# Performance work log

Measured on AMD Instinct MI355X. Metric: run time of the kernel, lower is better.

## Reference

```python
import jax, jax.numpy as jnp
import numpy as np

B, N, E = 16, 576, 768
H, HID = 12, 768
D = HID // H          # dim_head = 64
SCALE = D ** -0.5
LN_EPS = 1e-5


def setup_inputs() -> dict:
    key = jax.random.key(0)
    ks = jax.random.split(key, 12)
    x = jax.random.normal(ks[0], (B, N, E), jnp.float32)
    dist = jax.random.uniform(ks[1], (N, N), jnp.float32) * 24.0  # pairwise patch distances
    s = E ** -0.5
    return {
        "x": x,
        "dist": dist,
        "ln_g": jnp.ones((E,), jnp.float32),
        "ln_b": jnp.zeros((E,), jnp.float32),
        "Wq": jax.random.normal(ks[2], (E, HID), jnp.float32) * s,
        "bq": jnp.zeros((HID,), jnp.float32),
        "Wk": jax.random.normal(ks[3], (E, HID), jnp.float32) * s,
        "bk": jnp.zeros((HID,), jnp.float32),
        "Wv": jax.random.normal(ks[4], (E, HID), jnp.float32) * s,
        "bv": jnp.zeros((HID,), jnp.float32),
        "Wo": jax.random.normal(ks[5], (HID, E), jnp.float32) * (HID ** -0.5),
        "bo": jnp.zeros((E,), jnp.float32),
        "ak": jax.random.normal(ks[6], (D,), jnp.float32) * 0.1,
        "av": jax.random.normal(ks[7], (D,), jnp.float32) * 0.1,
    }


def _rpe(a, dist):
    # MonotonicallyDecreasingFunctionParallel: per-channel learned decay rate,
    # out[i,j,c] = exp(-softplus(a_c) * dist[i,j])  ->  [N, N, D]
    rate = jax.nn.softplus(a)
    return jnp.exp(-dist[:, :, None] * rate[None, None, :])


def reference(x, dist, ln_g, ln_b, Wq, bq, Wk, bk, Wv, bv, Wo, bo, ak, av):
    b, n = x.shape[0], x.shape[1]
    # LayerNorm
    mu = jnp.mean(x, axis=-1, keepdims=True)
    var = jnp.mean(jnp.square(x - mu), axis=-1, keepdims=True)
    xn = (x - mu) * jax.lax.rsqrt(var + LN_EPS) * ln_g + ln_b
    # projections, then raw row-major reshape [B, H, n, d] (faithful to .view)
    q = (xn @ Wq + bq).reshape(b, H, n, D)
    k = (xn @ Wk + bk).reshape(b, H, n, D)
    v = (xn @ Wv + bv).reshape(b, H, n, D)
    QKT = jnp.einsum("bhnd,bhmd->bhnm", q, k)
    rel_k = _rpe(ak, dist)  # [n, n, D]
    rel_v = _rpe(av, dist)  # [n, n, D]
    # faithful raw reshape [B,H,n,d] -> [n, B*H, d]
    q_r = q.reshape(n, b * H, D)
    QAT = jnp.einsum("nbd,nmd->nbm", q_r, rel_k).reshape(b, H, n, n)
    attn = jax.nn.softmax((QKT + QAT) * SCALE, axis=-1)
    attn_V = jnp.einsum("bhnm,bhmd->bhnd", attn, v)
    attn_r = attn.reshape(n, b * H, n)
    attn_rel_v = jnp.einsum("nbm,nmd->nbd", attn_r, rel_v).reshape(b, H, n, D)
    out = (attn_V + attn_rel_v).reshape(b, n, HID)
    out = out @ Wo + bo  # dropout is identity in eval mode
    return out
```

## Files before the change

### kernel.cpp

```cpp
#include <hip/hip_runtime.h>
#include <hip/hip_fp16.h>

typedef _Float16 f16;
typedef _Float16 v8hf __attribute__((ext_vector_type(8)));
typedef float v4f __attribute__((ext_vector_type(4)));
typedef float v16f __attribute__((ext_vector_type(16)));
typedef unsigned int v4u __attribute__((ext_vector_type(4)));

#define NROW 9216
#define SZH ((size_t)NROW * 768)

__device__ __forceinline__ float softplus_f(float a) {
  return fmaxf(a, 0.f) + log1pf(__expf(-fabsf(a)));
}

__device__ __forceinline__ unsigned int packh(float a, float b) {
  union { f16 h[2]; unsigned int u; } z;
  z.h[0] = (f16)a; z.h[1] = (f16)b;
  return z.u;
}

__global__ __launch_bounds__(256) void prep_kernel(
    const float* __restrict__ x, const float* __restrict__ lg, const float* __restrict__ lb,
    const float* __restrict__ Wq, const float* __restrict__ Wk, const float* __restrict__ Wv,
    const float* __restrict__ Wo, const float* __restrict__ ak, const float* __restrict__ av,
    const float* __restrict__ bq, const float* __restrict__ bk, const float* __restrict__ bv,
    f16* __restrict__ xn, f16* __restrict__ wt, float* __restrict__ biasqkv,
    float* __restrict__ rates)
{
  __shared__ float tile[64][65];
  __shared__ float red[8];
  int bid = blockIdx.x, tid = threadIdx.x;
  if (bid < NROW) {
    const float* xr = x + (size_t)bid * 768;
    float v0 = xr[tid], v1 = xr[tid + 256], v2 = xr[tid + 512];
    float s1 = v0 + v1 + v2;
    float s2 = v0 * v0 + v1 * v1 + v2 * v2;
    #pragma unroll
    for (int off = 32; off >= 1; off >>= 1) {
      s1 += __shfl_xor(s1, off);
      s2 += __shfl_xor(s2, off);
    }
    int w = tid >> 6;
    if ((tid & 63) == 0) { red[w] = s1; red[4 + w] = s2; }
    __syncthreads();
    s1 = red[0] + red[1] + red[2] + red[3];
    s2 = red[4] + red[5] + red[6] + red[7];
    float mu = s1 * (1.f / 768.f);
    float var = s2 * (1.f / 768.f) - mu * mu;
    float rs = rsqrtf(var + 1e-5f);
    f16* xo = xn + (size_t)bid * 768;
    xo[tid]       = (f16)((v0 - mu) * rs * lg[tid] + lb[tid]);
    xo[tid + 256] = (f16)((v1 - mu) * rs * lg[tid + 256] + lb[tid + 256]);
    xo[tid + 512] = (f16)((v2 - mu) * rs * lg[tid + 512] + lb[tid + 512]);
    return;
  }
  bid -= NROW;
  if (bid < 576) {
    int wsel = bid / 144, t2 = bid % 144, tr = t2 / 12, tc = t2 % 12;
    const float* W = (wsel == 0) ? Wq : ((wsel == 1) ? Wk : ((wsel == 2) ? Wv : Wo));
    f16* WT = wt + (size_t)wsel * 589824;
    int r = tid >> 2, c0 = (tid & 3) * 16;
    #pragma unroll
    for (int j = 0; j < 16; j++)
      tile[r][c0 + j] = W[(size_t)(tr * 64 + r) * 768 + tc * 64 + c0 + j];
    __syncthreads();
    #pragma unroll
    for (int j = 0; j < 16; j++)
      WT[(size_t)(tc * 64 + r) * 768 + tr * 64 + c0 + j] = (f16)tile[c0 + j][r];
    return;
  }
  if (tid < 64) rates[tid] = softplus_f(ak[tid]);
  else if (tid < 128) rates[tid] = softplus_f(av[tid - 64]);
  for (int i = tid; i < 2304; i += 256)
    biasqkv[i] = (i < 768) ? bq[i] : ((i < 1536) ? bk[i - 768] : bv[i - 1536]);
}

__global__ __launch_bounds__(256) void gemm_kernel(
    const f16* __restrict__ A, const f16* __restrict__ WT,
    const float* __restrict__ bias,
    f16* __restrict__ outh, float* __restrict__ outf, int f32out)
{
  __shared__ __align__(16) f16 At[128 * 64];
  __shared__ __align__(16) f16 Bt[128 * 64];
  int mb = blockIdx.x, nb = blockIdx.y;
  int tid = threadIdx.x, lane = tid & 63, w = tid >> 6;
  int wr = w >> 1, wc = w & 1;
  v4f acc[4][4];
  #pragma unroll
  for (int i = 0; i < 4; i++)
    #pragma unroll
    for (int j = 0; j < 4; j++) acc[i][j] = (v4f){0.f, 0.f, 0.f, 0.f};
  int arow0 = mb * 128, brow0 = nb * 128;
  for (int ks = 0; ks < 12; ++ks) {
    int k0 = ks * 64;
    #pragma unroll
    for (int qq = 0; qq < 4; ++qq) {
      int o = (qq * 256 + tid) * 16;
      int row = o >> 7, bc = o & 127;
      int dst = row * 128 + (bc ^ ((row & 7) << 4));
      *(v8hf*)((char*)At + dst) = *(const v8hf*)(A + (size_t)(arow0 + row) * 768 + k0 + (bc >> 1));
      *(v8hf*)((char*)Bt + dst) = *(const v8hf*)(WT + (size_t)(brow0 + row) * 768 + k0 + (bc >> 1));
    }
    __syncthreads();
    v8hf bf[4][2];
    #pragma unroll
    for (int cf = 0; cf < 4; cf++)
      #pragma unroll
      for (int kk = 0; kk < 2; kk++) {
        int row = wc * 64 + cf * 16 + (lane & 15);
        int bc = kk * 64 + ((lane >> 4) << 4);
        bf[cf][kk] = *(const v8hf*)((char*)Bt + row * 128 + (bc ^ ((row & 7) << 4)));
      }
    #pragma unroll
    for (int rf = 0; rf < 4; rf++) {
      v8hf af[2];
      int row = wr * 64 + rf * 16 + (lane & 15);
      #pragma unroll
      for (int kk = 0; kk < 2; kk++) {
        int bc = kk * 64 + ((lane >> 4) << 4);
        af[kk] = *(const v8hf*)((char*)At + row * 128 + (bc ^ ((row & 7) << 4)));
      }
      #pragma unroll
      for (int cf = 0; cf < 4; cf++) {
        acc[rf][cf] = __builtin_amdgcn_mfma_f32_16x16x32_f16(af[0], bf[cf][0], acc[rf][cf], 0, 0, 0);
        acc[rf][cf] = __builtin_amdgcn_mfma_f32_16x16x32_f16(af[1], bf[cf][1], acc[rf][cf], 0, 0, 0);
      }
    }
    __syncthreads();
  }
  #pragma unroll
  for (int cf = 0; cf < 4; cf++) {
    int col = nb * 128 + wc * 64 + cf * 16 + (lane & 15);
    float bb = bias[col];
    int z = col / 768;
    int colz = col - z * 768;
    #pragma unroll
    for (int rf = 0; rf < 4; rf++) {
      int row0 = mb * 128 + wr * 64 + rf * 16 + ((lane >> 4) << 2);
      #pragma unroll
      for (int r = 0; r < 4; r++) {
        float val = acc[rf][cf][r] + bb;
        if (f32out) outf[(size_t)(row0 + r) * 768 + col] = val;
        else outh[(size_t)z * SZH + (size_t)(row0 + r) * 768 + colz] = (f16)val;
      }
    }
  }
}

__global__ __launch_bounds__(256) void vt_kernel(const f16* __restrict__ vw, f16* __restrict__ vt)
{
  __shared__ f16 tile[64][72];
  int g = blockIdx.x, tc = blockIdx.y;
  int tid = threadIdx.x;
  int tr = tid >> 2, c16 = (tid & 3) * 16;
  const f16* src = vw + (size_t)g * 36864 + (size_t)(tc * 64 + tr) * 64 + c16;
  *(v8hf*)&tile[tr][c16] = *(const v8hf*)src;
  *(v8hf*)&tile[tr][c16 + 8] = *(const v8hf*)(src + 8);
  __syncthreads();
  int d = tid >> 2, t16 = (tid & 3) * 16;
  f16 outv[16];
  #pragma unroll
  for (int j = 0; j < 16; j++) outv[j] = tile[t16 + j][d];
  f16* dst = vt + (size_t)g * 36864 + (size_t)d * 576 + tc * 64 + t16;
  *(v8hf*)dst = *(v8hf*)outv;
  *(v8hf*)(dst + 8) = *(v8hf*)(outv + 8);
}

__global__ __launch_bounds__(384, 3) void attn_kernel(
    const f16* __restrict__ qw, const f16* __restrict__ kw, const f16* __restrict__ vt,
    const float* __restrict__ dist, const float* __restrict__ rates,
    f16* __restrict__ aw, float* __restrict__ part, float* __restrict__ ml, int nslice)
{
  __shared__ __align__(16) f16 Ke[64 * 64];
  __shared__ __align__(16) f16 Vt[64 * 64];
  __shared__ float dl[576];
  __shared__ float rkv[128];
  int gc = blockIdx.x;
  int sl = blockIdx.y;
  int g = gc / 3, c = gc - g * 3;
  int tid = threadIdx.x, lane = tid & 63, w = tid >> 6;
  int l31 = lane & 31, h = lane >> 5;
  int ntile = 9 / nslice;
  size_t hbase = (size_t)g * 36864;
  if (tid < 128) rkv[tid] = rates[tid];
  for (int t = tid; t < ntile * 64; t += 384)
    dl[t] = dist[(size_t)gc * 576 + sl * ntile * 64 + t];
  __syncthreads();
  v8hf qf[4];
  {
    const f16* qp = qw + hbase + (size_t)(c * 192 + w * 32 + l31) * 64 + h * 8;
    #pragma unroll
    for (int kk = 0; kk < 4; kk++) {
      v8hf v = *(const v8hf*)(qp + kk * 16);
      #pragma unroll
      for (int j = 0; j < 8; j++) v[j] = v[j] * (f16)0.125f;
      qf[kk] = v;
    }
  }
  v16f o0 = {0}, o1 = {0};
  #pragma unroll
  for (int i = 0; i < 16; i++) { o0[i] = 0.f; o1[i] = 0.f; }
  float mrun = -1e30f, lrun = 0.f;
  for (int t = 0; t < ntile; ++t) {
    int mbase = sl * ntile * 64 + t * 64;
    int mloc = t * 64;
    for (int u = tid; u < 1024; u += 384) {
      if (u < 512) {
        int mm = u >> 3, d8 = (u & 7) * 8;
        float dv = dl[mloc + mm];
        v8hf kv = *(const v8hf*)(kw + hbase + (size_t)(mbase + mm) * 64 + d8);
        #pragma unroll
        for (int j = 0; j < 8; j++)
          kv[j] = (f16)((float)kv[j] + __expf(-rkv[d8 + j] * dv));
        *(v8hf*)((char*)Ke + mm * 128 + ((d8 * 2) ^ ((mm & 7) << 4))) = kv;
      } else {
        int uu = u - 512;
        int dd = uu >> 3, m8 = (uu & 7) * 8;
        float rv = rkv[64 + dd];
        v8hf vv = *(const v8hf*)(vt + hbase + (size_t)dd * 576 + mbase + m8);
        #pragma unroll
        for (int j = 0; j < 8; j++)
          vv[j] = (f16)((float)vv[j] + __expf(-rv * dl[mloc + m8 + j]));
        *(v8hf*)((char*)Vt + dd * 128 + ((m8 * 2) ^ ((dd & 7) << 4))) = vv;
      }
    }
    __syncthreads();
    v16f s0 = {0}, s1 = {0};
    #pragma unroll
    for (int i = 0; i < 16; i++) { s0[i] = 0.f; s1[i] = 0.f; }
    #pragma unroll
    for (int kk = 0; kk < 4; kk++) {
      int bc = kk * 32 + h * 16;
      int sw0 = (l31 & 7) << 4;
      v8hf a0 = *(const v8hf*)((char*)Ke + l31 * 128 + (bc ^ sw0));
      v8hf a1 = *(const v8hf*)((char*)Ke + (32 + l31) * 128 + (bc ^ sw0));
      s0 = __builtin_amdgcn_mfma_f32_32x32x16_f16(a0, qf[kk], s0, 0, 0, 0);
      s1 = __builtin_amdgcn_mfma_f32_32x32x16_f16(a1, qf[kk], s1, 0, 0, 0);
    }
    float tmax = s0[0];
    #pragma unroll
    for (int i = 1; i < 16; i++) tmax = fmaxf(tmax, s0[i]);
    #pragma unroll
    for (int i = 0; i < 16; i++) tmax = fmaxf(tmax, s1[i]);
    tmax = fmaxf(tmax, __shfl_xor(tmax, 32));
    float mnew = fmaxf(mrun, tmax);
    float alpha = __expf(mrun - mnew);
    float rs = 0.f;
    #pragma unroll
    for (int i = 0; i < 16; i++) { float p = __expf(s0[i] - mnew); s0[i] = p; rs += p; }
    #pragma unroll
    for (int i = 0; i < 16; i++) { float p = __expf(s1[i] - mnew); s1[i] = p; rs += p; }
    rs += __shfl_xor(rs, 32);
    lrun = lrun * alpha + rs;
    mrun = mnew;
    #pragma unroll
    for (int i = 0; i < 16; i++) { o0[i] *= alpha; o1[i] *= alpha; }
    unsigned int Wd[16], Xd[16];
    #pragma unroll
    for (int i = 0; i < 8; i++) {
      Wd[i]     = packh(s0[2 * i], s0[2 * i + 1]);
      Wd[8 + i] = packh(s1[2 * i], s1[2 * i + 1]);
    }
    #pragma unroll
    for (int i = 0; i < 16; i++) Xd[i] = __shfl_xor((int)Wd[i], 32);
    v4u fw[4];
    fw[0] = h ? (v4u){Xd[2],  Xd[3],  Wd[2],  Wd[3]}  : (v4u){Wd[0],  Wd[1],  Xd[0],  Xd[1]};
    fw[1] = h ? (v4u){Xd[6],  Xd[7],  Wd[6],  Wd[7]}  : (v4u){Wd[4],  Wd[5],  Xd[4],  Xd[5]};
    fw[2] = h ? (v4u){Xd[10], Xd[11], Wd[10], Wd[11]} : (v4u){Wd[8],  Wd[9],  Xd[8],  Xd[9]};
    fw[3] = h ? (v4u){Xd[14], Xd[15], Wd[14], Wd[15]} : (v4u){Wd[12], Wd[13], Xd[12], Xd[13]};
    #pragma unroll
    for (int kk = 0; kk < 4; kk++) {
      int bc = kk * 32 + h * 16;
      int sw0 = (l31 & 7) << 4;
      v8hf a0 = *(const v8hf*)((char*)Vt + l31 * 128 + (bc ^ sw0));
      v8hf a1 = *(const v8hf*)((char*)Vt + (32 + l31) * 128 + (bc ^ sw0));
      union { v4u u; v8hf hh; } pb;
      pb.u = fw[kk];
      o0 = __builtin_amdgcn_mfma_f32_32x32x16_f16(a0, pb.hh, o0, 0, 0, 0);
      o1 = __builtin_amdgcn_mfma_f32_32x32x16_f16(a1, pb.hh, o1, 0, 0, 0);
    }
    __syncthreads();
  }
  if (nslice == 1) {
    float inv = 1.f / lrun;
    f16* ap = aw + hbase + (size_t)(c * 192 + w * 32 + l31) * 64;
    #pragma unroll
    for (int r = 0; r < 16; r++) {
      int d = (r & 3) + 8 * (r >> 2) + 4 * h;
      ap[d]      = (f16)(o0[r] * inv);
      ap[d + 32] = (f16)(o1[r] * inv);
    }
  } else {
    float* pp = part + ((size_t)sl * 576 + gc) * 12288;
    int q = w * 32 + l31;
    #pragma unroll
    for (int r = 0; r < 16; r++) {
      int d = (r & 3) + 8 * (r >> 2) + 4 * h;
      pp[d * 192 + q]        = o0[r];
      pp[(d + 32) * 192 + q] = o1[r];
    }
    if (h == 0) {
      float* mlp = ml + ((size_t)sl * 576 + gc) * 384;
      mlp[q]       = mrun;
      mlp[192 + q] = lrun;
    }
  }
}

__global__ __launch_bounds__(192) void comb_kernel(
    const float* __restrict__ part, const float* __restrict__ ml, f16* __restrict__ aw)
{
  int gc = blockIdx.x;
  int q = threadIdx.x;
  int g = gc / 3, c = gc - g * 3;
  float mv[3], lv[3];
  float M = -1e30f;
  #pragma unroll
  for (int s = 0; s < 3; s++) {
    const float* mlp = ml + ((size_t)s * 576 + gc) * 384;
    mv[s] = mlp[q];
    lv[s] = mlp[192 + q];
    M = fmaxf(M, mv[s]);
  }
  float L = 0.f, sc[3];
  #pragma unroll
  for (int s = 0; s < 3; s++) { sc[s] = __expf(mv[s] - M); L += lv[s] * sc[s]; }
  float inv = 1.f / L;
  f16 row[64];
  #pragma unroll
  for (int d = 0; d < 64; d++) {
    float a = 0.f;
    #pragma unroll
    for (int s = 0; s < 3; s++)
      a += part[((size_t)s * 576 + gc) * 12288 + d * 192 + q] * sc[s];
    row[d] = (f16)(a * inv);
  }
  f16* ap = aw + (size_t)g * 36864 + (size_t)(c * 192 + q) * 64;
  #pragma unroll
  for (int j = 0; j < 8; j++) *(v8hf*)(ap + j * 8) = *(v8hf*)(row + j * 8);
}

extern "C" void kernel_launch(void* const* d_in, const int* in_sizes, int n_in,
                              void* d_out, int out_size, void* d_ws, size_t ws_size,
                              hipStream_t stream) {
  const float* x    = (const float*)d_in[0];
  const float* dist = (const float*)d_in[1];
  const float* lg   = (const float*)d_in[2];
  const float* lb   = (const float*)d_in[3];
  const float* Wq   = (const float*)d_in[4];
  const float* bq   = (const float*)d_in[5];
  const float* Wk   = (const float*)d_in[6];
  const float* bk   = (const float*)d_in[7];
  const float* Wv   = (const float*)d_in[8];
  const float* bv   = (const float*)d_in[9];
  const float* Wo   = (const float*)d_in[10];
  const float* bo   = (const float*)d_in[11];
  const float* ak   = (const float*)d_in[12];
  const float* av   = (const float*)d_in[13];

  f16* ws = (f16*)d_ws;
  f16* xn = ws;
  f16* qw = ws + SZH;
  f16* kw = ws + 2 * SZH;
  f16* vw = ws + 3 * SZH;
  f16* wt = ws + 4 * SZH;
  float* fbase   = (float*)(ws + 4 * SZH + 4 * 589824);
  float* biasqkv = fbase;
  float* rates   = fbase + 2304;
  float* part    = fbase + 2432;
  float* mlb     = part + (size_t)3 * 576 * 12288;
  f16* vtb = xn;
  f16* aw  = vw;

  size_t need_split = ((size_t)(4 * SZH + 4 * 589824) * 2) + 4 * (2432 + (size_t)3 * 576 * 12288 + (size_t)3 * 576 * 384);
  int ns = (ws_size >= need_split) ? 3 : 1;

  prep_kernel<<<9216 + 576 + 1, 256, 0, stream>>>(x, lg, lb, Wq, Wk, Wv, Wo, ak, av,
                                                  bq, bk, bv, xn, wt, biasqkv, rates);
  gemm_kernel<<<dim3(72, 18), 256, 0, stream>>>(xn, wt, biasqkv, qw, nullptr, 0);
  vt_kernel<<<dim3(192, 9), 256, 0, stream>>>(vw, vtb);
  attn_kernel<<<dim3(576, ns), 384, 0, stream>>>(qw, kw, vtb, dist, rates, aw, part, mlb, ns);
  if (ns > 1)
    comb_kernel<<<576, 192, 0, stream>>>(part, mlb, aw);
  gemm_kernel<<<dim3(72, 6), 256, 0, stream>>>(aw, wt + 3 * 589824, bo, nullptr, (float*)d_out, 1);
}
```

Baseline: 189.4 us.

## Use direct global-to-LDS loads, XCD-aware block remap, lazy softmax rescale, fp16 partials

The GEMM tile loads now use global_load_lds DMA instead of going through registers, and GEMM and attention workgroup indices are remapped so neighbouring tiles land on the same XCD. The online softmax skips the max and accumulator rescale unless the new tile max exceeds the running max by more than 8, which saves exponentials and multiplies. Split-K attention partials are normalised and stored as fp16 instead of fp32, halving combine traffic at some cost in precision. packh also switches to the cvt_pkrtz intrinsic.

```diff
diff --git a/kernel.cpp b/kernel.cpp
--- a/kernel.cpp
+++ b/kernel.cpp
@@ -3,6 +3,7 @@
 
 typedef _Float16 f16;
 typedef _Float16 v8hf __attribute__((ext_vector_type(8)));
+typedef __fp16 v2fp __attribute__((ext_vector_type(2)));
 typedef float v4f __attribute__((ext_vector_type(4)));
 typedef float v16f __attribute__((ext_vector_type(16)));
 typedef unsigned int v4u __attribute__((ext_vector_type(4)));
@@ -15,9 +16,16 @@
 }
 
 __device__ __forceinline__ unsigned int packh(float a, float b) {
-  union { f16 h[2]; unsigned int u; } z;
-  z.h[0] = (f16)a; z.h[1] = (f16)b;
+  union { v2fp h; unsigned int u; } z;
+  z.h = __builtin_amdgcn_cvt_pkrtz(a, b);
   return z.u;
+}
+
+__device__ __forceinline__ void gload16(const void* g, void* l) {
+  __builtin_amdgcn_global_load_lds(
+      (const __attribute__((address_space(1))) unsigned int*)(unsigned long long)g,
+      (__attribute__((address_space(3))) unsigned int*)(unsigned int)(unsigned long long)l,
+      16, 0, 0);
 }
 
 __global__ __launch_bounds__(256) void prep_kernel(
@@ -83,7 +91,11 @@
 {
   __shared__ __align__(16) f16 At[128 * 64];
   __shared__ __align__(16) f16 Bt[128 * 64];
-  int mb = blockIdx.x, nb = blockIdx.y;
+  int bid0 = blockIdx.y * gridDim.x + blockIdx.x;
+  int nwg = gridDim.x * gridDim.y;
+  int nid = (bid0 & 7) * (nwg >> 3) + (bid0 >> 3);
+  int cols = gridDim.y;
+  int mb = nid / cols, nb = nid % cols;
   int tid = threadIdx.x, lane = tid & 63, w = tid >> 6;
   int wr = w >> 1, wc = w & 1;
   v4f acc[4][4];
@@ -92,15 +104,16 @@
     #pragma unroll
     for (int j = 0; j < 4; j++) acc[i][j] = (v4f){0.f, 0.f, 0.f, 0.f};
   int arow0 = mb * 128, brow0 = nb * 128;
+  int rb = w * 32 + (lane >> 3);
+  int ch = lane & 7;
   for (int ks = 0; ks < 12; ++ks) {
     int k0 = ks * 64;
     #pragma unroll
-    for (int qq = 0; qq < 4; ++qq) {
-      int o = (qq * 256 + tid) * 16;
-      int row = o >> 7, bc = o & 127;
-      int dst = row * 128 + (bc ^ ((row & 7) << 4));
-      *(v8hf*)((char*)At + dst) = *(const v8hf*)(A + (size_t)(arow0 + row) * 768 + k0 + (bc >> 1));
-      *(v8hf*)((char*)Bt + dst) = *(const v8hf*)(WT + (size_t)(brow0 + row) * 768 + k0 + (bc >> 1));
+    for (int j = 0; j < 4; j++) {
+      int row = rb + j * 8;
+      int sc = ((ch ^ (row & 7)) << 3);
+      gload16(A  + (size_t)(arow0 + row) * 768 + k0 + sc, (char*)At + w * 4096 + j * 1024);
+      gload16(WT + (size_t)(brow0 + row) * 768 + k0 + sc, (char*)Bt + w * 4096 + j * 1024);
     }
     __syncthreads();
     v8hf bf[4][2];
@@ -170,13 +183,13 @@
 __global__ __launch_bounds__(384, 3) void attn_kernel(
     const f16* __restrict__ qw, const f16* __restrict__ kw, const f16* __restrict__ vt,
     const float* __restrict__ dist, const float* __restrict__ rates,
-    f16* __restrict__ aw, float* __restrict__ part, float* __restrict__ ml, int nslice)
+    f16* __restrict__ aw, f16* __restrict__ parth, float* __restrict__ ml, int nslice)
 {
   __shared__ __align__(16) f16 Ke[64 * 64];
   __shared__ __align__(16) f16 Vt[64 * 64];
   __shared__ float dl[576];
   __shared__ float rkv[128];
-  int gc = blockIdx.x;
+  int gc = (blockIdx.x & 7) * 72 + (blockIdx.x >> 3);
   int sl = blockIdx.y;
   int g = gc / 3, c = gc - g * 3;
   int tid = threadIdx.x, lane = tid & 63, w = tid >> 6;
@@ -198,7 +211,7 @@
       qf[kk] = v;
     }
   }
-  v16f o0 = {0}, o1 = {0};
+  v16f o0, o1;
   #pragma unroll
   for (int i = 0; i < 16; i++) { o0[i] = 0.f; o1[i] = 0.f; }
   float mrun = -1e30f, lrun = 0.f;
@@ -226,7 +239,7 @@
       }
     }
     __syncthreads();
-    v16f s0 = {0}, s1 = {0};
+    v16f s0, s1;
     #pragma unroll
     for (int i = 0; i < 16; i++) { s0[i] = 0.f; s1[i] = 0.f; }
     #pragma unroll
@@ -244,18 +257,21 @@
     #pragma unroll
     for (int i = 0; i < 16; i++) tmax = fmaxf(tmax, s1[i]);
     tmax = fmaxf(tmax, __shfl_xor(tmax, 32));
-    float mnew = fmaxf(mrun, tmax);
-    float alpha = __expf(mrun - mnew);
+    if (!__all(tmax - mrun <= 8.f)) {
+      float mnew = fmaxf(mrun, tmax);
+      float alpha = __expf(mrun - mnew);
+      lrun *= alpha;
+      #pragma unroll
+      for (int i = 0; i < 16; i++) { o0[i] *= alpha; o1[i] *= alpha; }
+      mrun = mnew;
+    }
     float rs = 0.f;
     #pragma unroll
-    for (int i = 0; i < 16; i++) { float p = __expf(s0[i] - mnew); s0[i] = p; rs += p; }
-    #pragma unroll
-    for (int i = 0; i < 16; i++) { float p = __expf(s1[i] - mnew); s1[i] = p; rs += p; }
+    for (int i = 0; i < 16; i++) { float p = __expf(s0[i] - mrun); s0[i] = p; rs += p; }
+    #pragma unroll
+    for (int i = 0; i < 16; i++) { float p = __expf(s1[i] - mrun); s1[i] = p; rs += p; }
     rs += __shfl_xor(rs, 32);
-    lrun = lrun * alpha + rs;
-    mrun = mnew;
-    #pragma unroll
-    for (int i = 0; i < 16; i++) { o0[i] *= alpha; o1[i] *= alpha; }
+    lrun += rs;
     unsigned int Wd[16], Xd[16];
     #pragma unroll
     for (int i = 0; i < 8; i++) {
@@ -282,8 +298,8 @@
     }
     __syncthreads();
   }
+  float inv = 1.f / lrun;
   if (nslice == 1) {
-    float inv = 1.f / lrun;
     f16* ap = aw + hbase + (size_t)(c * 192 + w * 32 + l31) * 64;
     #pragma unroll
     for (int r = 0; r < 16; r++) {
@@ -292,13 +308,13 @@
       ap[d + 32] = (f16)(o1[r] * inv);
     }
   } else {
-    float* pp = part + ((size_t)sl * 576 + gc) * 12288;
+    f16* pp = parth + ((size_t)sl * 576 + gc) * 12288;
     int q = w * 32 + l31;
     #pragma unroll
     for (int r = 0; r < 16; r++) {
       int d = (r & 3) + 8 * (r >> 2) + 4 * h;
-      pp[d * 192 + q]        = o0[r];
-      pp[(d + 32) * 192 + q] = o1[r];
+      pp[d * 192 + q]        = (f16)(o0[r] * inv);
+      pp[(d + 32) * 192 + q] = (f16)(o1[r] * inv);
     }
     if (h == 0) {
       float* mlp = ml + ((size_t)sl * 576 + gc) * 384;
@@ -309,7 +325,7 @@
 }
 
 __global__ __launch_bounds__(192) void comb_kernel(
-    const float* __restrict__ part, const float* __restrict__ ml, f16* __restrict__ aw)
+    const f16* __restrict__ parth, const float* __restrict__ ml, f16* __restrict__ aw)
 {
   int gc = blockIdx.x;
   int q = threadIdx.x;
@@ -323,18 +339,20 @@
     lv[s] = mlp[192 + q];
     M = fmaxf(M, mv[s]);
   }
-  float L = 0.f, sc[3];
-  #pragma unroll
-  for (int s = 0; s < 3; s++) { sc[s] = __expf(mv[s] - M); L += lv[s] * sc[s]; }
-  float inv = 1.f / L;
+  float L = 0.f, wgt[3];
+  #pragma unroll
+  for (int s = 0; s < 3; s++) { wgt[s] = lv[s] * __expf(mv[s] - M); L += wgt[s]; }
+  float invL = 1.f / L;
+  #pragma unroll
+  for (int s = 0; s < 3; s++) wgt[s] *= invL;
   f16 row[64];
   #pragma unroll
   for (int d = 0; d < 64; d++) {
     float a = 0.f;
     #pragma unroll
     for (int s = 0; s < 3; s++)
-      a += part[((size_t)s * 576 + gc) * 12288 + d * 192 + q] * sc[s];
-    row[d] = (f16)(a * inv);
+      a += wgt[s] * (float)parth[((size_t)s * 576 + gc) * 12288 + d * 192 + q];
+    row[d] = (f16)a;
   }
   f16* ap = aw + (size_t)g * 36864 + (size_t)(c * 192 + q) * 64;
   #pragma unroll
@@ -365,23 +383,24 @@
   f16* kw = ws + 2 * SZH;
   f16* vw = ws + 3 * SZH;
   f16* wt = ws + 4 * SZH;
-  float* fbase   = (float*)(ws + 4 * SZH + 4 * 589824);
+  float* fbase   = (float*)(wt + 4 * 589824);
   float* biasqkv = fbase;
   float* rates   = fbase + 2304;
-  float* part    = fbase + 2432;
-  float* mlb     = part + (size_t)3 * 576 * 12288;
+  f16* parth     = (f16*)(fbase + 2432);
+  float* mlb     = (float*)(parth + (size_t)3 * 576 * 12288);
   f16* vtb = xn;
   f16* aw  = vw;
 
-  size_t need_split = ((size_t)(4 * SZH + 4 * 589824) * 2) + 4 * (2432 + (size_t)3 * 576 * 12288 + (size_t)3 * 576 * 384);
+  size_t need_split = ((size_t)4 * SZH + 4 * 589824 + (size_t)3 * 576 * 12288) * 2
+                    + ((size_t)2432 + (size_t)3 * 576 * 384) * 4;
   int ns = (ws_size >= need_split) ? 3 : 1;
 
   prep_kernel<<<9216 + 576 + 1, 256, 0, stream>>>(x, lg, lb, Wq, Wk, Wv, Wo, ak, av,
                                                   bq, bk, bv, xn, wt, biasqkv, rates);
   gemm_kernel<<<dim3(72, 18), 256, 0, stream>>>(xn, wt, biasqkv, qw, nullptr, 0);
   vt_kernel<<<dim3(192, 9), 256, 0, stream>>>(vw, vtb);
-  attn_kernel<<<dim3(576, ns), 384, 0, stream>>>(qw, kw, vtb, dist, rates, aw, part, mlb, ns);
+  attn_kernel<<<dim3(576, ns), 384, 0, stream>>>(qw, kw, vtb, dist, rates, aw, parth, mlb, ns);
   if (ns > 1)
-    comb_kernel<<<576, 192, 0, stream>>>(part, mlb, aw);
+    comb_kernel<<<576, 192, 0, stream>>>(parth, mlb, aw);
   gemm_kernel<<<dim3(72, 6), 256, 0, stream>>>(aw, wt + 3 * 589824, bo, nullptr, (float*)d_out, 1);
 }
```

Result: faster. 169.6 us (-10.4%).
